# Performance work log

Hardware: AMD Instinct MI355X
Metric: run time of the kernel (lower is better)

The kernel has to match this reference:

```python
import jax, jax.numpy as jnp
import numpy as np

B, C, H, W = 8, 64, 64, 64
T, G, HID = 8, 8, 64


def setup_inputs() -> dict:
    key = jax.random.key(0)
    ks = jax.random.split(key, 8)
    s = 0.05
    return {
        "h": jax.random.normal(ks[0], (B, C, H, W), jnp.float32),
        "w_in": jax.random.normal(ks[1], (G * T, C), jnp.float32) * s,
        "b_in": jnp.zeros((G * T,), jnp.float32),
        "w_ih": jax.random.normal(ks[2], (4 * HID, 1), jnp.float32) * s,
        "w_hh": jax.random.normal(ks[3], (4 * HID, HID), jnp.float32) * s,
        "b_ih": jnp.zeros((4 * HID,), jnp.float32),
        "b_hh": jnp.zeros((4 * HID,), jnp.float32),
        "w_s": jax.random.normal(ks[4], (1, HID), jnp.float32) * s,
        "b_s": jnp.zeros((1,), jnp.float32),
        "w_out": jax.random.normal(ks[5], (C, G * T), jnp.float32) * s,
        "b_out": jnp.zeros((C,), jnp.float32),
    }


def reference(h, w_in, b_in, w_ih, w_hh, b_ih, b_hh, w_s, b_s, w_out, b_out):
    Bb, Cc, Hh, Ww = h.shape
    # 1x1 conv in-projection: (B,C,H,W) -> (B,G*T,H,W)
    y = jnp.einsum('bchw,oc->bohw', h, w_in) + b_in[None, :, None, None]
    y = y.reshape(Bb, G, T, Hh, Ww)
    # (B,G,H,W,T) -> (N,T) scalar sequences
    seq = jnp.transpose(y, (0, 1, 3, 4, 2)).reshape(-1, T)
    N = seq.shape[0]
    xs = seq.T  # (T, N) time-major for scan
    bias = b_ih + b_hh  # (4H,)
    w_x = w_ih[:, 0]    # (4H,) scalar-input weights

    def step(carry, x_t):
        hprev, cprev = carry
        # gates: i, f, g, o in torch LSTM ordering
        gates = x_t[:, None] * w_x[None, :] + hprev @ w_hh.T + bias  # (N,4H)
        i, f, g, o = jnp.split(gates, 4, axis=1)
        i = jax.nn.sigmoid(i)
        f = jax.nn.sigmoid(f)
        o = jax.nn.sigmoid(o)
        g = jnp.tanh(g)
        c = f * cprev + i * g
        hn = o * jnp.tanh(c)
        s_t = hn @ w_s[0] + b_s[0]  # fused to_scalar: (N,)
        return (hn, c), s_t

    init = (jnp.zeros((N, HID), h.dtype), jnp.zeros((N, HID), h.dtype))
    _, s = jax.lax.scan(step, init, xs)  # s: (T, N)

    out = s.T.reshape(Bb, G, Hh, Ww, T)
    out = jnp.transpose(out, (0, 1, 4, 2, 3)).reshape(Bb, G * T, Hh, Ww)
    # 1x1 conv out-projection back to C channels
    out = jnp.einsum('bchw,oc->bohw', out, w_out) + b_out[None, :, None, None]
    return out
```

## Files before the change

kernel.cpp:

```cpp
#include <hip/hip_runtime.h>
#include <hip/hip_bf16.h>

#define HW    4096
#define BB    8
#define TT    8

constexpr int OFF_SBUF  = 0;
constexpr int OFF_WFRAG = 2097152;
constexpr int OFF_WTOUT = OFF_WFRAG + 8704;
constexpr int OFF_WXB   = OFF_WTOUT + 4096;

typedef _Float16 halfx8 __attribute__((ext_vector_type(8)));
typedef float    floatx4 __attribute__((ext_vector_type(4)));
typedef float    floatx2 __attribute__((ext_vector_type(2)));

__device__ inline float fast_exp2(float x) {
#if __has_builtin(__builtin_amdgcn_exp2f)
    return __builtin_amdgcn_exp2f(x);
#else
    return __builtin_exp2f(x);
#endif
}
__device__ inline float fast_rcp(float x) {
#if __has_builtin(__builtin_amdgcn_rcpf)
    return __builtin_amdgcn_rcpf(x);
#else
    return 1.0f / x;
#endif
}
__device__ inline floatx2 exp2x2(floatx2 x) {
    floatx2 r; r.x = fast_exp2(x.x); r.y = fast_exp2(x.y); return r;
}
__device__ inline floatx2 rcpx2(floatx2 x) {
    floatx2 r; r.x = fast_rcp(x.x); r.y = fast_rcp(x.y); return r;
}
__device__ inline floatx2 fsig2(floatx2 x) {
    return rcpx2(exp2x2(x * -1.44269504088896f) + 1.0f);
}
__device__ inline floatx2 ftanh2(floatx2 x) {
    floatx2 r = rcpx2(exp2x2(x * 2.88539008177793f) + 1.0f);
    return r * -2.0f + 1.0f;
}

union pack8 { _Float16 h[8]; uint4 u; };

__global__ __launch_bounds__(256) void prep_kernel(
    const float* __restrict__ w_ih,  const float* __restrict__ w_hh,
    const float* __restrict__ b_ih,  const float* __restrict__ b_hh,
    const float* __restrict__ w_s,   const float* __restrict__ w_out,
    float* __restrict__ ws_f) {
    int tid = threadIdx.x;
    if (blockIdx.x == 0) {
        uint4* wf = (uint4*)(ws_f + OFF_WFRAG);
        #pragma unroll
        for (int i = 0; i < 8; ++i) {
            int e  = tid + 256 * i;
            int l  = e & 63;
            int fi = e >> 6;
            int nb = fi >> 1, kc = fi & 1;
            int gate = (l & 15) + 16 * nb;
            int hid  = kc * 32 + (l >> 4) * 8;
            const float* src = w_hh + gate * 64 + hid;
            pack8 p;
            #pragma unroll
            for (int j = 0; j < 8; ++j) p.h[j] = (_Float16)src[j];
            wf[e] = p.u;
        }
        if (tid < 128) {
            int l = tid & 63, kc = tid >> 6;
            pack8 p;
            #pragma unroll
            for (int j = 0; j < 8; ++j) p.h[j] = (_Float16)0.0f;
            if ((l & 15) == 0) {
                #pragma unroll
                for (int j = 0; j < 8; ++j)
                    p.h[j] = (_Float16)w_s[kc * 32 + (l >> 4) * 8 + j];
            }
            wf[2048 + kc * 64 + l] = p.u;
        }
    } else {
        #pragma unroll
        for (int i = 0; i < 16; ++i) {
            int idx = tid + 256 * i;
            int o = idx & 63, c = idx >> 6;
            ws_f[OFF_WTOUT + idx] = w_out[o * 64 + c];
        }
        floatx2* wxb = (floatx2*)(ws_f + OFF_WXB);
        floatx2 v; v.x = w_ih[tid]; v.y = b_ih[tid] + b_hh[tid];
        wxb[tid] = v;
    }
}

__global__ __launch_bounds__(512) void lstm_kernel(
    const float* __restrict__ hin,
    const float* __restrict__ ws_f,
    float* __restrict__ s_buf,
    const float* __restrict__ w_in,
    const float* __restrict__ b_in,
    const float* __restrict__ b_s_p) {
    __shared__ uint4 wfrag_lds[2176];
    __shared__ floatx2 wxb_lds[256];
    __shared__ floatx2 w8p[256];
    __shared__ __align__(16) unsigned char uni[32768];
    float*    h_stage = (float*)uni;
    float*    x_lds   = (float*)uni;
    _Float16* h_lds   = (_Float16*)(uni + 4096);

    int tid = threadIdx.x;
    int bg    = blockIdx.x & 63;
    int ptile = blockIdx.x >> 6;
    int b = bg >> 3, g = bg & 7;
    int p0 = ptile * 128;

    int lane = tid & 63;
    int wv   = tid >> 6;
    int s    = lane & 15;
    int q    = lane >> 4;

    const uint4* wfg = (const uint4*)(ws_f + OFF_WFRAG);
    #pragma unroll
    for (int i = 0; i < 5; ++i) {
        int e = tid + 512 * i;
        if (e < 2176) wfrag_lds[e] = wfg[e];
    }
    if (tid < 256) {
        wxb_lds[tid] = ((const floatx2*)(ws_f + OFF_WXB))[tid];
        int c = tid >> 2, tq_ = tid & 3;
        floatx2 v;
        v.x = w_in[(g * 8 + tq_) * 64 + c];
        v.y = w_in[(g * 8 + tq_ + 4) * 64 + c];
        w8p[tid] = v;
    }

    #pragma unroll
    for (int i = 0; i < 4; ++i) {
        int e  = tid + 512 * i;
        int cc = e >> 5, f4 = e & 31;
        ((floatx4*)h_stage)[e] = *(const floatx4*)&hin[(b * 64 + cc) * HW + p0 + f4 * 4];
    }
    __syncthreads();

    int px = tid & 127, tq = tid >> 7;
    floatx2 xacc; xacc.x = b_in[g * 8 + tq]; xacc.y = b_in[g * 8 + tq + 4];
    #pragma unroll 8
    for (int cc = 0; cc < 64; ++cc) {
        float hv = h_stage[cc * 128 + px];
        floatx2 w = w8p[cc * 4 + tq];
        floatx2 h2; h2.x = hv; h2.y = hv;
        xacc = xacc + w * h2;
    }
    __syncthreads();
    x_lds[tq * 128 + px]       = xacc.x;
    x_lds[(tq + 4) * 128 + px] = xacc.y;
    #pragma unroll
    for (int i = 0; i < 9; ++i)
        ((unsigned*)(uni + 4096))[tid + 512 * i] = 0u;
    __syncthreads();

    _Float16* hrow = h_lds + wv * 16 * 72;
    int pw = p0 + wv * 16;
    float bs = b_s_p[0];

    float c_st[4][4];
    #pragma unroll
    for (int hb = 0; hb < 4; ++hb)
        #pragma unroll
        for (int r = 0; r < 4; ++r) c_st[hb][r] = 0.0f;

    for (int t = 0; t < TT; ++t) {
        asm volatile("" ::: "memory");

        halfx8 a0 = *(const halfx8*)(hrow + s * 72 + q * 8);
        halfx8 a1 = *(const halfx8*)(hrow + s * 72 + q * 8 + 32);

        if (t > 0) {
            halfx8 sb0 = *(const halfx8*)&wfrag_lds[32 * 64 + lane];
            halfx8 sb1 = *(const halfx8*)&wfrag_lds[33 * 64 + lane];
            floatx4 sa = {0.f, 0.f, 0.f, 0.f};
            sa = __builtin_amdgcn_mfma_f32_16x16x32_f16(a0, sb0, sa, 0, 0, 0);
            sa = __builtin_amdgcn_mfma_f32_16x16x32_f16(a1, sb1, sa, 0, 0, 0);
            if (s == 0) {
                floatx4 o4 = {sa[0] + bs, sa[1] + bs, sa[2] + bs, sa[3] + bs};
                *(floatx4*)&s_buf[(bg * 8 + (t - 1)) * HW + pw + q * 4] = o4;
            }
        }

        floatx4 xv = *(const floatx4*)&x_lds[t * 128 + wv * 16 + q * 4];
        floatx2 xlo; xlo.x = xv[0]; xlo.y = xv[1];
        floatx2 xhi; xhi.x = xv[2]; xhi.y = xv[3];

        #pragma unroll
        for (int hb = 0; hb < 4; ++hb) {
            floatx4 acc[4];
            #pragma unroll
            for (int gi = 0; gi < 4; ++gi) {
                int nb = hb + 4 * gi;
                floatx2 wb = wxb_lds[s + 16 * nb];
                floatx2 lo = xlo * wb.x + wb.y;
                floatx2 hi = xhi * wb.x + wb.y;
                floatx4 a = {lo.x, lo.y, hi.x, hi.y};
                halfx8 b0 = *(const halfx8*)&wfrag_lds[(nb * 2 + 0) * 64 + lane];
                halfx8 b1 = *(const halfx8*)&wfrag_lds[(nb * 2 + 1) * 64 + lane];
                a = __builtin_amdgcn_mfma_f32_16x16x32_f16(a0, b0, a, 0, 0, 0);
                a = __builtin_amdgcn_mfma_f32_16x16x32_f16(a1, b1, a, 0, 0, 0);
                acc[gi] = a;
            }
            int s16 = s + 16 * hb;
            _Float16* wp = hrow + (q * 4) * 72 + s16;
            #pragma unroll
            for (int p = 0; p < 2; ++p) {
                int r0 = 2 * p;
                floatx2 iv; iv.x = acc[0][r0]; iv.y = acc[0][r0 + 1]; iv = fsig2(iv);
                floatx2 fv; fv.x = acc[1][r0]; fv.y = acc[1][r0 + 1]; fv = fsig2(fv);
                floatx2 gv; gv.x = acc[2][r0]; gv.y = acc[2][r0 + 1]; gv = ftanh2(gv);
                floatx2 ov; ov.x = acc[3][r0]; ov.y = acc[3][r0 + 1]; ov = fsig2(ov);
                floatx2 cp; cp.x = c_st[hb][r0]; cp.y = c_st[hb][r0 + 1];
                floatx2 c = fv * cp + iv * gv;
                c_st[hb][r0] = c.x; c_st[hb][r0 + 1] = c.y;
                floatx2 hn = ov * ftanh2(c);
                wp[(r0 + 0) * 72] = (_Float16)hn.x;
                wp[(r0 + 1) * 72] = (_Float16)hn.y;
            }
        }
    }
    {
        asm volatile("" ::: "memory");
        halfx8 a0 = *(const halfx8*)(hrow + s * 72 + q * 8);
        halfx8 a1 = *(const halfx8*)(hrow + s * 72 + q * 8 + 32);
        halfx8 sb0 = *(const halfx8*)&wfrag_lds[32 * 64 + lane];
        halfx8 sb1 = *(const halfx8*)&wfrag_lds[33 * 64 + lane];
        floatx4 sa = {0.f, 0.f, 0.f, 0.f};
        sa = __builtin_amdgcn_mfma_f32_16x16x32_f16(a0, sb0, sa, 0, 0, 0);
        sa = __builtin_amdgcn_mfma_f32_16x16x32_f16(a1, sb1, sa, 0, 0, 0);
        if (s == 0) {
            floatx4 o4 = {sa[0] + bs, sa[1] + bs, sa[2] + bs, sa[3] + bs};
            *(floatx4*)&s_buf[(bg * 8 + 7) * HW + pw + q * 4] = o4;
        }
    }
}

__global__ __launch_bounds__(256) void conv_out_kernel(
    const float* __restrict__ x, const float* __restrict__ Wt,
    const float* __restrict__ bias, float* __restrict__ y) {
    int p  = blockIdx.x * 256 + threadIdx.x;
    int b  = blockIdx.y;
    int oh = blockIdx.z;
    const float* xb = x + b * 64 * HW;
    const floatx2* Wt2 = (const floatx2*)Wt;
    floatx2 acc[4];
    #pragma unroll
    for (int j = 0; j < 4; ++j) { acc[j].x = 0.f; acc[j].y = 0.f; }
    #pragma unroll 8
    for (int c = 0; c < 64; ++c) {
        float hv = xb[c * HW + p];
        floatx2 h2; h2.x = hv; h2.y = hv;
        #pragma unroll
        for (int j = 0; j < 4; ++j)
            acc[j] = acc[j] + Wt2[c * 32 + oh * 4 + j] * h2;
    }
    float* yb = y + b * 64 * HW + oh * 8 * HW;
    #pragma unroll
    for (int j = 0; j < 4; ++j) {
        yb[(2 * j) * HW + p]     = acc[j].x + bias[oh * 8 + 2 * j];
        yb[(2 * j + 1) * HW + p] = acc[j].y + bias[oh * 8 + 2 * j + 1];
    }
}

extern "C" void kernel_launch(void* const* d_in, const int* in_sizes, int n_in,
                              void* d_out, int out_size, void* d_ws, size_t ws_size,
                              hipStream_t stream) {
    const float* h     = (const float*)d_in[0];
    const float* w_in  = (const float*)d_in[1];
    const float* b_in  = (const float*)d_in[2];
    const float* w_ih  = (const float*)d_in[3];
    const float* w_hh  = (const float*)d_in[4];
    const float* b_ih  = (const float*)d_in[5];
    const float* b_hh  = (const float*)d_in[6];
    const float* w_s   = (const float*)d_in[7];
    const float* b_s   = (const float*)d_in[8];
    const float* w_out = (const float*)d_in[9];
    const float* b_out = (const float*)d_in[10];
    float* out = (float*)d_out;
    float* ws  = (float*)d_ws;

    prep_kernel<<<2, 256, 0, stream>>>(w_ih, w_hh, b_ih, b_hh, w_s, w_out, ws);
    lstm_kernel<<<2048, 512, 0, stream>>>(h, ws, ws + OFF_SBUF, w_in, b_in, b_s);
    conv_out_kernel<<<dim3(16, BB, 8), 256, 0, stream>>>(ws + OFF_SBUF, ws + OFF_WTOUT, b_out, out);
}
```

Baseline: 246.3 us.

## Fuse output 1x1 conv into LSTM kernel and retile blocks by pixel

```diff
diff --git a/kernel.cpp b/kernel.cpp
--- a/kernel.cpp
+++ b/kernel.cpp
@@ -5,8 +5,7 @@
 #define BB    8
 #define TT    8
 
-constexpr int OFF_SBUF  = 0;
-constexpr int OFF_WFRAG = 2097152;
+constexpr int OFF_WFRAG = 0;
 constexpr int OFF_WTOUT = OFF_WFRAG + 8704;
 constexpr int OFF_WXB   = OFF_WTOUT + 4096;
 
@@ -94,26 +93,26 @@
 __global__ __launch_bounds__(512) void lstm_kernel(
     const float* __restrict__ hin,
     const float* __restrict__ ws_f,
-    float* __restrict__ s_buf,
+    float* __restrict__ out,
     const float* __restrict__ w_in,
     const float* __restrict__ b_in,
-    const float* __restrict__ b_s_p) {
+    const float* __restrict__ b_s_p,
+    const float* __restrict__ b_out) {
     __shared__ uint4 wfrag_lds[2176];
     __shared__ floatx2 wxb_lds[256];
-    __shared__ floatx2 w8p[256];
-    __shared__ __align__(16) unsigned char uni[32768];
-    float*    h_stage = (float*)uni;
-    float*    x_lds   = (float*)uni;
-    _Float16* h_lds   = (_Float16*)(uni + 4096);
+    __shared__ __align__(16) float x_lds[1024];
+    __shared__ __align__(16) _Float16 h_lds[9216];
+    __shared__ __align__(16) float stile[1024];
+    __shared__ __align__(16) float wt_lds[4096];
 
     int tid = threadIdx.x;
-    int bg    = blockIdx.x & 63;
-    int ptile = blockIdx.x >> 6;
-    int b = bg >> 3, g = bg & 7;
-    int p0 = ptile * 128;
+    int ptile = blockIdx.x & 255;
+    int b     = blockIdx.x >> 8;
+    int p0 = ptile * 16;
 
     int lane = tid & 63;
     int wv   = tid >> 6;
+    int g    = wv;
     int s    = lane & 15;
     int q    = lane >> 4;
 
@@ -123,42 +122,41 @@
         int e = tid + 512 * i;
         if (e < 2176) wfrag_lds[e] = wfg[e];
     }
+    if (tid < 256) wxb_lds[tid] = ((const floatx2*)(ws_f + OFF_WXB))[tid];
+    #pragma unroll
+    for (int i = 0; i < 2; ++i)
+        ((floatx4*)wt_lds)[tid + 512 * i] = ((const floatx4*)w_in)[tid + 512 * i];
     if (tid < 256) {
-        wxb_lds[tid] = ((const floatx2*)(ws_f + OFF_WXB))[tid];
-        int c = tid >> 2, tq_ = tid & 3;
-        floatx2 v;
-        v.x = w_in[(g * 8 + tq_) * 64 + c];
-        v.y = w_in[(g * 8 + tq_ + 4) * 64 + c];
-        w8p[tid] = v;
-    }
-
-    #pragma unroll
-    for (int i = 0; i < 4; ++i) {
-        int e  = tid + 512 * i;
-        int cc = e >> 5, f4 = e & 31;
-        ((floatx4*)h_stage)[e] = *(const floatx4*)&hin[(b * 64 + cc) * HW + p0 + f4 * 4];
+        int cc = tid >> 2, f4 = tid & 3;
+        ((floatx4*)stile)[tid] = *(const floatx4*)&hin[(b * 64 + cc) * HW + p0 + f4 * 4];
     }
     __syncthreads();
 
-    int px = tid & 127, tq = tid >> 7;
-    floatx2 xacc; xacc.x = b_in[g * 8 + tq]; xacc.y = b_in[g * 8 + tq + 4];
-    #pragma unroll 8
-    for (int cc = 0; cc < 64; ++cc) {
-        float hv = h_stage[cc * 128 + px];
-        floatx2 w = w8p[cc * 4 + tq];
-        floatx2 h2; h2.x = hv; h2.y = hv;
-        xacc = xacc + w * h2;
-    }
+    {
+        floatx2 xacc; xacc.x = b_in[g * 8 + q]; xacc.y = b_in[g * 8 + q + 4];
+        #pragma unroll 8
+        for (int cc = 0; cc < 64; ++cc) {
+            float hv = stile[cc * 16 + s];
+            floatx2 w;
+            w.x = wt_lds[(g * 8 + q) * 64 + cc];
+            w.y = wt_lds[(g * 8 + q + 4) * 64 + cc];
+            floatx2 h2; h2.x = hv; h2.y = hv;
+            xacc = xacc + w * h2;
+        }
+        x_lds[g * 128 + q * 16 + s]       = xacc.x;
+        x_lds[g * 128 + (q + 4) * 16 + s] = xacc.y;
+    }
+    #pragma unroll
+    for (int i = 0; i < 9; ++i)
+        ((unsigned*)h_lds)[tid + 512 * i] = 0u;
     __syncthreads();
-    x_lds[tq * 128 + px]       = xacc.x;
-    x_lds[(tq + 4) * 128 + px] = xacc.y;
-    #pragma unroll
-    for (int i = 0; i < 9; ++i)
-        ((unsigned*)(uni + 4096))[tid + 512 * i] = 0u;
-    __syncthreads();
+
+    #pragma unroll
+    for (int i = 0; i < 2; ++i)
+        ((floatx4*)wt_lds)[tid + 512 * i] =
+            ((const floatx4*)(ws_f + OFF_WTOUT))[tid + 512 * i];
 
     _Float16* hrow = h_lds + wv * 16 * 72;
-    int pw = p0 + wv * 16;
     float bs = b_s_p[0];
 
     float c_st[4][4];
@@ -181,11 +179,11 @@
             sa = __builtin_amdgcn_mfma_f32_16x16x32_f16(a1, sb1, sa, 0, 0, 0);
             if (s == 0) {
                 floatx4 o4 = {sa[0] + bs, sa[1] + bs, sa[2] + bs, sa[3] + bs};
-                *(floatx4*)&s_buf[(bg * 8 + (t - 1)) * HW + pw + q * 4] = o4;
-            }
-        }
-
-        floatx4 xv = *(const floatx4*)&x_lds[t * 128 + wv * 16 + q * 4];
+                *(floatx4*)&stile[(g * 8 + (t - 1)) * 16 + q * 4] = o4;
+            }
+        }
+
+        floatx4 xv = *(const floatx4*)&x_lds[g * 128 + t * 16 + q * 4];
         floatx2 xlo; xlo.x = xv[0]; xlo.y = xv[1];
         floatx2 xhi; xhi.x = xv[2]; xhi.y = xv[3];
 
@@ -234,35 +232,26 @@
         sa = __builtin_amdgcn_mfma_f32_16x16x32_f16(a1, sb1, sa, 0, 0, 0);
         if (s == 0) {
             floatx4 o4 = {sa[0] + bs, sa[1] + bs, sa[2] + bs, sa[3] + bs};
-            *(floatx4*)&s_buf[(bg * 8 + 7) * HW + pw + q * 4] = o4;
-        }
-    }
-}
-
-__global__ __launch_bounds__(256) void conv_out_kernel(
-    const float* __restrict__ x, const float* __restrict__ Wt,
-    const float* __restrict__ bias, float* __restrict__ y) {
-    int p  = blockIdx.x * 256 + threadIdx.x;
-    int b  = blockIdx.y;
-    int oh = blockIdx.z;
-    const float* xb = x + b * 64 * HW;
-    const floatx2* Wt2 = (const floatx2*)Wt;
-    floatx2 acc[4];
-    #pragma unroll
-    for (int j = 0; j < 4; ++j) { acc[j].x = 0.f; acc[j].y = 0.f; }
-    #pragma unroll 8
-    for (int c = 0; c < 64; ++c) {
-        float hv = xb[c * HW + p];
-        floatx2 h2; h2.x = hv; h2.y = hv;
-        #pragma unroll
-        for (int j = 0; j < 4; ++j)
-            acc[j] = acc[j] + Wt2[c * 32 + oh * 4 + j] * h2;
-    }
-    float* yb = y + b * 64 * HW + oh * 8 * HW;
-    #pragma unroll
-    for (int j = 0; j < 4; ++j) {
-        yb[(2 * j) * HW + p]     = acc[j].x + bias[oh * 8 + 2 * j];
-        yb[(2 * j + 1) * HW + p] = acc[j].y + bias[oh * 8 + 2 * j + 1];
+            *(floatx4*)&stile[(g * 8 + 7) * 16 + q * 4] = o4;
+        }
+    }
+    __syncthreads();
+
+    {
+        int px = tid & 15;
+        int oo = tid >> 4;
+        floatx2 acc; acc.x = b_out[oo]; acc.y = b_out[oo + 32];
+        #pragma unroll 8
+        for (int c = 0; c < 64; ++c) {
+            float sv = stile[c * 16 + px];
+            floatx2 w;
+            w.x = wt_lds[c * 64 + oo];
+            w.y = wt_lds[c * 64 + oo + 32];
+            floatx2 s2; s2.x = sv; s2.y = sv;
+            acc = acc + w * s2;
+        }
+        out[(b * 64 + oo) * HW + p0 + px]      = acc.x;
+        out[(b * 64 + oo + 32) * HW + p0 + px] = acc.y;
     }
 }
 
@@ -284,6 +273,5 @@
     float* ws  = (float*)d_ws;
 
     prep_kernel<<<2, 256, 0, stream>>>(w_ih, w_hh, b_ih, b_hh, w_s, w_out, ws);
-    lstm_kernel<<<2048, 512, 0, stream>>>(h, ws, ws + OFF_SBUF, w_in, b_in, b_s);
-    conv_out_kernel<<<dim3(16, BB, 8), 256, 0, stream>>>(ws + OFF_SBUF, ws + OFF_WTOUT, b_out, out);
-}
+    lstm_kernel<<<2048, 512, 0, stream>>>(h, ws, out, w_in, b_in, b_s, b_out);
+}
```

After: 244.8 us. About the same (-0.6%).
